# Performance work log

Measured on AMD Instinct MI355X. Metric: run time of the kernel, lower is better.

The kernel has to match this reference:

```python
import jax, jax.numpy as jnp
import numpy as np
from jax import lax

F8 = jnp.float8_e4m3fn


def setup_inputs() -> dict:
    key = jax.random.key(0)
    kx, kw = jax.random.split(key)
    x = jax.random.normal(kx, (2, 128, 4, 192, 320), dtype=jnp.float32)
    # matches reset_parameters: normal(0, 0.02) then cast to fp8
    weight = jax.random.normal(kw, (128, 128, 3, 3, 3), dtype=jnp.float32) * 0.02
    return {"x": x, "weight": weight}


def reference(x, weight):
    # fp8 e4m3 quantization round-trip (the torch module stores/consumes fp8),
    # compute/accumulate in fp32 as an fp8 conv kernel would.
    xq = x.astype(F8).astype(jnp.float32)
    wq = weight.astype(F8).astype(jnp.float32)
    # causal temporal padding: (kT-1, 0) = (2, 0); spatial 'same' padding (1,1)
    xp = jnp.pad(xq, ((0, 0), (0, 0), (2, 0), (1, 1), (1, 1)))
    out = lax.conv_general_dilated(
        xp, wq,
        window_strides=(1, 1, 1),
        padding='VALID',
        dimension_numbers=('NCDHW', 'OIDHW', 'NCDHW'),
    )  # (B, 128, 4, 192, 320)
    return out
```

## Files before the change

### kernel.cpp

```cpp
#include <hip/hip_runtime.h>
#include <hip/hip_fp8.h>


using f32x16 = __attribute__((ext_vector_type(16))) float;
using i32x8 = __attribute__((ext_vector_type(8))) int;
using i32x4 = __attribute__((ext_vector_type(4))) int;
typedef long long i64;
struct alignas(16) L2v { i64 x, y; };

namespace {
constexpr int Cc = 128, Dd = 4, Hh = 192, Ww = 320;
constexpr int HP = 194, WP = 322;
constexpr int NTAP = 27;
constexpr size_t PLANE = (size_t)4 * WP * 32;
constexpr size_t XQ_BYTES = (size_t)2 * Dd * HP * PLANE;
constexpr int ZA = 8 * 2 * 2576;
constexpr int ZB = 8 * 192 * 32;
constexpr int GSTR = WP * 32;
constexpr int HB = 1056;
constexpr int BSTR = 4 * 4 * 2 * HB;
}

__global__ __launch_bounds__(256) void zero_pad_kernel(unsigned char* __restrict__ xq) {
  int i = blockIdx.x * 256 + threadIdx.x;
  if (i < ZA) {
    int bd = i / (2 * 2576);
    int r = i - bd * (2 * 2576);
    int hsel = r / 2576, seg = r - hsel * 2576;
    L2v z{0, 0};
    *(L2v*)(xq + ((size_t)bd * HP + (hsel ? 193 : 0)) * PLANE + (size_t)seg * 16) = z;
  } else if (i < ZA + ZB) {
    int j = i - ZA;
    int bd = j / (192 * 32);
    int r = j - bd * (192 * 32);
    int h = r / 32 + 1;
    int t = r & 31;
    int g = t >> 3, s2 = t & 7;
    int wsel = s2 >> 2, part = s2 & 3;
    *(i64*)(xq + ((size_t)bd * HP + h) * PLANE + (size_t)g * GSTR
            + (size_t)(wsel ? 321 : 0) * 32 + part * 8) = 0;
  }
}

__global__ __launch_bounds__(256) void qx_kernel(const float* __restrict__ x,
                                                 unsigned char* __restrict__ xq) {
  __shared__ unsigned char lt[64 * 136];
  const int tid = threadIdx.x;
  const int b = blockIdx.z >> 2, d = blockIdx.z & 3;
  const int h = blockIdx.y;
  const int w0 = blockIdx.x * 64;
  const int wl = tid & 63, cig = tid >> 6;
  const size_t cstr = (size_t)Dd * Hh * Ww;
  const float* xp = x + (((size_t)b * Cc * Dd + d) * Hh + h) * Ww + w0 + wl;
  #pragma unroll 4
  for (int i = 0; i < 32; ++i) {
    int ci = cig * 32 + i;
    __hip_fp8_e4m3 q(xp[ci * cstr]);
    lt[wl * 136 + ci] = q.__x;
  }
  __syncthreads();
  unsigned char* plane = xq + ((size_t)(b * Dd + d) * HP + h + 1) * PLANE;
  {
    int g = tid >> 6, w = tid & 63;
    const unsigned char* src = lt + w * 136 + g * 32;
    i64 a0 = *(const i64*)(src), a1 = *(const i64*)(src + 8);
    i64 a2 = *(const i64*)(src + 16), a3 = *(const i64*)(src + 24);
    unsigned char* dst = plane + (size_t)g * GSTR + (size_t)(w0 + 1 + w) * 32;
    *(L2v*)dst = L2v{a0, a1};
    *(L2v*)(dst + 16) = L2v{a2, a3};
  }
}

__global__ void wpack_kernel(const float* __restrict__ w, unsigned char* __restrict__ wpk) {
  int idx = blockIdx.x * 256 + threadIdx.x;
  if (idx >= Cc * Cc * NTAP) return;
  int tap = idx % NTAP;
  int t = idx / NTAP;
  int ci = t % Cc, co = t / Cc;
  int cc = ci >> 6, cq = co >> 5;
  int lane = (((ci >> 5) & 1) << 5) | (co & 31);
  __hip_fp8_e4m3 q(w[idx]);
  wpk[((((size_t)tap * 2 + cc) * 4 + cq) * 64 + lane) * 32 + (ci & 31)] = q.__x;
}

__global__ __launch_bounds__(256, 2) void conv_mfma(const unsigned char* __restrict__ xq,
                                                    const unsigned char* __restrict__ wpk,
                                                    float* __restrict__ out) {
  __shared__ unsigned char lb[2 * BSTR];
  const int tid = threadIdx.x;
  const int lane = tid & 63, wv = tid >> 6;
  const int l31 = lane & 31, chalf = lane >> 5;
  const int hr = wv >> 1, ch = wv & 1;
  const int id = blockIdx.x;
  const int xcd = id & 7, j = id >> 3;
  const int h0l = j / 20, rem = j - h0l * 20;
  const int wx = rem >> 2, dout = rem & 3;
  const int h0 = (xcd * 12 + h0l) * 2;
  const int w0 = wx * 64;
  const int kdmin = dout >= 2 ? 0 : 2 - dout;

  const unsigned char* bb[3];
  #pragma unroll
  for (int kw = 0; kw < 3; ++kw)
    bb[kw] = lb + (hr * 4 + chalf) * 2 * HB + (l31 + kw) * 16;

  f32x16 acc[2][2][2];
  #pragma unroll
  for (int s = 0; s < 2; ++s)
    #pragma unroll
    for (int a = 0; a < 2; ++a)
      #pragma unroll
      for (int n = 0; n < 2; ++n)
        #pragma unroll
        for (int r = 0; r < 16; ++r) acc[s][a][n][r] = 0.f;

  for (int kd = kdmin; kd < 3; ++kd) {
    __syncthreads();
    for (int u = tid; u < 2112; u += 256) {
      int w = u % 66, rest = u / 66;
      int bsel = rest >> 4, r = rest & 15;
      int g = r & 3, hrow = r >> 2;
      const unsigned char* src = xq
          + ((size_t)(bsel * Dd + dout + kd - 2) * HP + h0 + hrow) * PLANE
          + (size_t)g * GSTR + (size_t)(w0 + w) * 32;
      L2v lo = *(const L2v*)src;
      L2v hi = *(const L2v*)(src + 16);
      unsigned char* base = lb + bsel * BSTR + (hrow * 4 + g) * 2 * HB + w * 16;
      *(L2v*)(base) = lo;
      *(L2v*)(base + HB) = hi;
    }
    __syncthreads();
    __builtin_amdgcn_s_setprio(1);
    #pragma unroll
    for (int kh = 0; kh < 3; ++kh)
      #pragma unroll
      for (int cc = 0; cc < 2; ++cc)
        #pragma unroll
        for (int kw = 0; kw < 3; ++kw) {
          i32x8 av[2];
          #pragma unroll
          for (int ct = 0; ct < 2; ++ct)
            av[ct] = *(const i32x8*)(wpk +
                ((((size_t)((kd * 9 + kh * 3 + kw) * 2) + cc) * 4 + ch * 2 + ct) * 64 + lane) * 32);
          #pragma unroll
          for (int bsel = 0; bsel < 2; ++bsel)
            #pragma unroll
            for (int nf = 0; nf < 2; ++nf) {
              const int off = bsel * BSTR + (kh * 4 + cc * 2) * 2 * HB + nf * 512;
              i32x4 blo = *(const i32x4*)(bb[kw] + off);
              i32x4 bhi = *(const i32x4*)(bb[kw] + off + HB);
              i32x8 bv = __builtin_shufflevector(blo, bhi, 0, 1, 2, 3, 4, 5, 6, 7);
              #pragma unroll
              for (int ct = 0; ct < 2; ++ct)
                acc[bsel][ct][nf] = __builtin_amdgcn_mfma_scale_f32_32x32x64_f8f6f4(
                    av[ct], bv, acc[bsel][ct][nf], 0, 0, 0, 127, 0, 127);
            }
        }
    __builtin_amdgcn_s_setprio(0);
  }

  #pragma unroll
  for (int bsel = 0; bsel < 2; ++bsel)
    #pragma unroll
    for (int ct = 0; ct < 2; ++ct)
      #pragma unroll
      for (int nf = 0; nf < 2; ++nf) {
        int ww = w0 + nf * 32 + l31;
        #pragma unroll
        for (int reg = 0; reg < 16; ++reg) {
          int co = ch * 64 + ct * 32 + (reg & 3) + 8 * (reg >> 2) + 4 * chalf;
          out[(((size_t)bsel * Cc + co) * Dd + dout) * (size_t)(Hh * Ww)
              + (size_t)(h0 + hr) * Ww + ww] = acc[bsel][ct][nf][reg];
        }
      }
}

extern "C" void kernel_launch(void* const* d_in, const int* in_sizes, int n_in,
                              void* d_out, int out_size, void* d_ws, size_t ws_size,
                              hipStream_t stream) {
  const float* x = (const float*)d_in[0];
  const float* w = (const float*)d_in[1];
  unsigned char* xq = (unsigned char*)d_ws;
  unsigned char* wpk = xq + XQ_BYTES;
  float* out = (float*)d_out;

  int nz = ZA + ZB;
  zero_pad_kernel<<<(nz + 255) / 256, 256, 0, stream>>>(xq);

  dim3 g1(Ww / 64, Hh, 2 * Dd);
  qx_kernel<<<g1, 256, 0, stream>>>(x, xq);

  int nw = Cc * Cc * NTAP;
  wpack_kernel<<<(nw + 255) / 256, 256, 0, stream>>>(w, wpk);

  conv_mfma<<<dim3(1920), 256, 0, stream>>>(xq, wpk, out);
}
```

Measured before the change: 259.2 us.

## Retile conv blocks over 4 output rows of one batch and load via global_load_lds

```diff
diff --git a/kernel.cpp b/kernel.cpp
--- a/kernel.cpp
+++ b/kernel.cpp
@@ -18,7 +18,8 @@
 constexpr int ZB = 8 * 192 * 32;
 constexpr int GSTR = WP * 32;
 constexpr int HB = 1056;
-constexpr int BSTR = 4 * 4 * 2 * HB;
+constexpr int NU = 6 * 4 * 2 * 66;
+constexpr int KDSTR = 9 * 2 * 4 * 64 * 32;
 }
 
 __global__ __launch_bounds__(256) void zero_pad_kernel(unsigned char* __restrict__ xq) {
@@ -83,53 +84,63 @@
   wpk[((((size_t)tap * 2 + cc) * 4 + cq) * 64 + lane) * 32 + (ci & 31)] = q.__x;
 }
 
+__device__ __forceinline__ void gll16(const unsigned char* g, unsigned char* l) {
+  __builtin_amdgcn_global_load_lds(
+      (const __attribute__((address_space(1))) void*)g,
+      (__attribute__((address_space(3))) void*)l, 16, 0, 0);
+}
+
 __global__ __launch_bounds__(256, 2) void conv_mfma(const unsigned char* __restrict__ xq,
                                                     const unsigned char* __restrict__ wpk,
                                                     float* __restrict__ out) {
-  __shared__ unsigned char lb[2 * BSTR];
+  __shared__ unsigned char lb[48 * HB];
   const int tid = threadIdx.x;
   const int lane = tid & 63, wv = tid >> 6;
   const int l31 = lane & 31, chalf = lane >> 5;
   const int hr = wv >> 1, ch = wv & 1;
   const int id = blockIdx.x;
   const int xcd = id & 7, j = id >> 3;
-  const int h0l = j / 20, rem = j - h0l * 20;
-  const int wx = rem >> 2, dout = rem & 3;
-  const int h0 = (xcd * 12 + h0l) * 2;
+  const int h0l = j / 40, rem = j - h0l * 40;
+  const int z = rem / 5, wx = rem - z * 5;
+  const int b = z >> 2, dout = z & 3;
+  const int h0 = (xcd * 6 + h0l) * 4;
   const int w0 = wx * 64;
   const int kdmin = dout >= 2 ? 0 : 2 - dout;
+
+  const long imgstep = (long)HP * PLANE;
+  const long img0 = (long)(b * Dd + dout - 2) * imgstep;
+
+  const unsigned char* vbase = wpk + ch * 4096 + lane * 32;
 
   const unsigned char* bb[3];
   #pragma unroll
   for (int kw = 0; kw < 3; ++kw)
-    bb[kw] = lb + (hr * 4 + chalf) * 2 * HB + (l31 + kw) * 16;
+    bb[kw] = lb + hr * (2 * 8 * HB) + chalf * (2 * HB) + (l31 + kw) * 16;
 
   f32x16 acc[2][2][2];
   #pragma unroll
-  for (int s = 0; s < 2; ++s)
+  for (int hl = 0; hl < 2; ++hl)
     #pragma unroll
     for (int a = 0; a < 2; ++a)
       #pragma unroll
       for (int n = 0; n < 2; ++n)
         #pragma unroll
-        for (int r = 0; r < 16; ++r) acc[s][a][n][r] = 0.f;
+        for (int r = 0; r < 16; ++r) acc[hl][a][n][r] = 0.f;
 
   for (int kd = kdmin; kd < 3; ++kd) {
     __syncthreads();
-    for (int u = tid; u < 2112; u += 256) {
-      int w = u % 66, rest = u / 66;
-      int bsel = rest >> 4, r = rest & 15;
-      int g = r & 3, hrow = r >> 2;
-      const unsigned char* src = xq
-          + ((size_t)(bsel * Dd + dout + kd - 2) * HP + h0 + hrow) * PLANE
-          + (size_t)g * GSTR + (size_t)(w0 + w) * 32;
-      L2v lo = *(const L2v*)src;
-      L2v hi = *(const L2v*)(src + 16);
-      unsigned char* base = lb + bsel * BSTR + (hrow * 4 + g) * 2 * HB + w * 16;
-      *(L2v*)(base) = lo;
-      *(L2v*)(base + HB) = hi;
+    const unsigned char* img = xq + img0 + (long)kd * imgstep;
+    for (int u = tid; u < NU; u += 256) {
+      int w = u % 66;
+      int rest = u / 66;
+      int half = rest & 1, rg = rest >> 1;
+      int g = rg & 3, hrow = rg >> 2;
+      gll16(img + (size_t)(h0 + hrow) * PLANE + (size_t)g * GSTR
+                + (size_t)(w0 + w) * 32 + half * 16,
+            lb + u * 16);
     }
     __syncthreads();
+
     __builtin_amdgcn_s_setprio(1);
     #pragma unroll
     for (int kh = 0; kh < 3; ++kh)
@@ -140,27 +151,27 @@
           i32x8 av[2];
           #pragma unroll
           for (int ct = 0; ct < 2; ++ct)
-            av[ct] = *(const i32x8*)(wpk +
-                ((((size_t)((kd * 9 + kh * 3 + kw) * 2) + cc) * 4 + ch * 2 + ct) * 64 + lane) * 32);
+            av[ct] = *(const i32x8*)(vbase + (size_t)kd * KDSTR
+                + ((kh * 3 + kw) * 2 + cc) * 8192 + ct * 2048);
           #pragma unroll
-          for (int bsel = 0; bsel < 2; ++bsel)
+          for (int hl = 0; hl < 2; ++hl)
             #pragma unroll
             for (int nf = 0; nf < 2; ++nf) {
-              const int off = bsel * BSTR + (kh * 4 + cc * 2) * 2 * HB + nf * 512;
+              const int off = (hl + kh) * (8 * HB) + cc * (4 * HB) + nf * 512;
               i32x4 blo = *(const i32x4*)(bb[kw] + off);
               i32x4 bhi = *(const i32x4*)(bb[kw] + off + HB);
               i32x8 bv = __builtin_shufflevector(blo, bhi, 0, 1, 2, 3, 4, 5, 6, 7);
               #pragma unroll
               for (int ct = 0; ct < 2; ++ct)
-                acc[bsel][ct][nf] = __builtin_amdgcn_mfma_scale_f32_32x32x64_f8f6f4(
-                    av[ct], bv, acc[bsel][ct][nf], 0, 0, 0, 127, 0, 127);
+                acc[hl][ct][nf] = __builtin_amdgcn_mfma_scale_f32_32x32x64_f8f6f4(
+                    av[ct], bv, acc[hl][ct][nf], 0, 0, 0, 127, 0, 127);
             }
         }
     __builtin_amdgcn_s_setprio(0);
   }
 
   #pragma unroll
-  for (int bsel = 0; bsel < 2; ++bsel)
+  for (int hl = 0; hl < 2; ++hl)
     #pragma unroll
     for (int ct = 0; ct < 2; ++ct)
       #pragma unroll
@@ -169,8 +180,8 @@
         #pragma unroll
         for (int reg = 0; reg < 16; ++reg) {
           int co = ch * 64 + ct * 32 + (reg & 3) + 8 * (reg >> 2) + 4 * chalf;
-          out[(((size_t)bsel * Cc + co) * Dd + dout) * (size_t)(Hh * Ww)
-              + (size_t)(h0 + hr) * Ww + ww] = acc[bsel][ct][nf][reg];
+          out[(((size_t)b * Cc + co) * Dd + dout) * (size_t)(Hh * Ww)
+              + (size_t)(h0 + hr * 2 + hl) * Ww + ww] = acc[hl][ct][nf][reg];
         }
       }
 }
```

Result: slower. 473.4 us (+82.7%).
